# Optimization experiments

Measured on AMD Instinct MI355X. Metric: run time of the kernel, lower is better.

## Reference

```python
import jax, jax.numpy as jnp
import numpy as np

B, S, D, E, H = 8, 1024, 1024, 8, 4096  # batch, seq, n_embd, num_experts, 4*n_embd


def setup_inputs() -> dict:
    key = jax.random.key(0)
    ks = jax.random.split(key, 8)
    sc = 0.02
    return {
        "x": jax.random.normal(ks[0], (B, S, D), jnp.float32),
        "noise": jax.random.normal(ks[1], (B, S, E), jnp.float32),
        "Wg": jax.random.normal(ks[2], (D, E), jnp.float32) * sc,
        "bg": jnp.zeros((E,), jnp.float32),
        "Wn": jax.random.normal(ks[3], (D, E), jnp.float32) * sc,
        "bn": jnp.zeros((E,), jnp.float32),
        "W1": jax.random.normal(ks[4], (E, D, H), jnp.float32) * sc,
        "b1": jnp.zeros((E, H), jnp.float32),
        "W2": jax.random.normal(ks[5], (E, H, D), jnp.float32) * sc,
        "b2": jnp.zeros((E, D), jnp.float32),
        "top_k": 2,
    }


def reference(x, noise, Wg, bg, Wn, bn, W1, b1, W2, b2, top_k):
    # --- NoisyTopkRouter ---
    logits = jnp.einsum("bsd,de->bse", x, Wg) + bg
    noise_logits = jnp.einsum("bsd,de->bse", x, Wn) + bn
    noisy = logits + noise * jax.nn.softplus(noise_logits)  # [B,S,E]
    _, idx = jax.lax.top_k(noisy, top_k)  # [B,S,K]
    in_topk = jax.nn.one_hot(idx, noisy.shape[-1], dtype=noisy.dtype).sum(-2) > 0
    sparse_logits = jnp.where(in_topk, noisy, -jnp.inf)
    gating = jax.nn.softmax(sparse_logits, axis=-1)  # zero outside top-k

    # --- dispatch/combine: gating is exactly zero for non-selected experts,
    # so per-expert masked gather + weighted scatter-add == gated dense sum ---
    g_e = jnp.moveaxis(gating, -1, 0)  # [E,B,S]

    def body(acc, params):
        W1e, b1e, W2e, b2e, ge = params
        h = jax.nn.relu(jnp.einsum("bsd,dh->bsh", x, W1e) + b1e)  # [B,S,H]
        y = (jnp.einsum("bsh,hd->bsd", h, W2e) + b2e) * ge[..., None]
        return acc + y, y

    final_output, expert_outputs = jax.lax.scan(
        body, jnp.zeros_like(x), (W1, b1, W2, b2, g_e)
    )
    # expert_outputs: [E,B,S,D], matching the per-expert weighted outputs list
    return final_output, expert_outputs, gating
```

## Files before the change

kernel.cpp:

```cpp
#include <hip/hip_runtime.h>
#include <hip/hip_bf16.h>
#include <stdint.h>

#define TKN   8192
#define DD    1024
#define EE    8
#define HH    4096
#define TOPK  2
#define NASG  (TKN * TOPK)

typedef unsigned short u16;
typedef __bf16 bf16x8 __attribute__((ext_vector_type(8)));
typedef float  f32x4  __attribute__((ext_vector_type(4)));

__device__ __forceinline__ u16 f2bf(float f) {
  __hip_bfloat16 h = __float2bfloat16(f);
  return __builtin_bit_cast(u16, h);
}

__device__ __forceinline__ void glds16(const void* g, void* l) {
  __builtin_amdgcn_global_load_lds(
      (__attribute__((address_space(1))) void*)g,
      (__attribute__((address_space(3))) void*)l, 16, 0, 0);
}

#define FENCE() asm volatile("" ::: "memory")
#define BAR()   do { FENCE(); __builtin_amdgcn_s_barrier(); FENCE(); } while (0)
#define VMCNT4() asm volatile("s_waitcnt vmcnt(4)" ::: "memory")
#define VMCNT0() asm volatile("s_waitcnt vmcnt(0)" ::: "memory")

__global__ __launch_bounds__(256) void transpose_cvt_kernel(
    const float* __restrict__ src, u16* __restrict__ dst, int R, int C) {
  __shared__ float tile[32][33];
  int e = blockIdx.z;
  int c0 = blockIdx.x * 32, r0 = blockIdx.y * 32;
  int tx = threadIdx.x, ty = threadIdx.y;
  const float* s = src + (size_t)e * R * C;
  u16* d = dst + (size_t)e * R * C;
#pragma unroll
  for (int j = 0; j < 4; j++)
    tile[ty * 4 + j][tx] = s[(size_t)(r0 + ty * 4 + j) * C + c0 + tx];
  __syncthreads();
#pragma unroll
  for (int j = 0; j < 4; j++)
    d[(size_t)(c0 + ty * 4 + j) * R + r0 + tx] = f2bf(tile[tx][ty * 4 + j]);
}

__global__ __launch_bounds__(256) void router_kernel(
    const float* __restrict__ x, const float* __restrict__ noise,
    const float* __restrict__ Wg, const float* __restrict__ bg,
    const float* __restrict__ Wn, const float* __restrict__ bn,
    float* __restrict__ gating, u16* __restrict__ xb,
    int* __restrict__ sel_e, float* __restrict__ sel_g) {
  int t = blockIdx.x;
  int tid = threadIdx.x;
  float acc[16];
#pragma unroll
  for (int j = 0; j < 16; j++) acc[j] = 0.f;
  for (int i = tid; i < DD; i += 256) {
    float xv = x[(size_t)t * DD + i];
    xb[(size_t)t * DD + i] = f2bf(xv);
    const float4* g4 = (const float4*)(Wg + (size_t)i * EE);
    const float4* n4 = (const float4*)(Wn + (size_t)i * EE);
    float4 ga = g4[0], gb = g4[1];
    float4 na = n4[0], nb = n4[1];
    acc[0] += xv * ga.x;  acc[1] += xv * ga.y;  acc[2] += xv * ga.z;  acc[3] += xv * ga.w;
    acc[4] += xv * gb.x;  acc[5] += xv * gb.y;  acc[6] += xv * gb.z;  acc[7] += xv * gb.w;
    acc[8] += xv * na.x;  acc[9] += xv * na.y;  acc[10] += xv * na.z; acc[11] += xv * na.w;
    acc[12] += xv * nb.x; acc[13] += xv * nb.y; acc[14] += xv * nb.z; acc[15] += xv * nb.w;
  }
  __shared__ float red[4][16];
  int lane = tid & 63, wv = tid >> 6;
#pragma unroll
  for (int j = 0; j < 16; j++) {
    float v = acc[j];
    for (int o = 32; o > 0; o >>= 1) v += __shfl_down(v, o);
    acc[j] = v;
  }
  if (lane == 0) {
#pragma unroll
    for (int j = 0; j < 16; j++) red[wv][j] = acc[j];
  }
  __syncthreads();
  if (tid == 0) {
    float nz[EE];
#pragma unroll
    for (int e = 0; e < EE; e++) {
      float dg = red[0][e] + red[1][e] + red[2][e] + red[3][e] + bg[e];
      float dn = red[0][8 + e] + red[1][8 + e] + red[2][8 + e] + red[3][8 + e] + bn[e];
      float sp = fmaxf(dn, 0.f) + log1pf(expf(-fabsf(dn)));
      nz[e] = dg + noise[(size_t)t * EE + e] * sp;
    }
    int m1 = 0;
    for (int e = 1; e < EE; e++) if (nz[e] > nz[m1]) m1 = e;
    int m2 = (m1 == 0) ? 1 : 0;
    for (int e = 0; e < EE; e++) if (e != m1 && nz[e] > nz[m2]) m2 = e;
    float eb = expf(nz[m2] - nz[m1]);
    float den = 1.f + eb;
    float g1 = 1.f / den, g2 = eb / den;
    gating[(size_t)t * EE + m1] = g1;
    gating[(size_t)t * EE + m2] = g2;
    sel_e[t * 2] = m1; sel_e[t * 2 + 1] = m2;
    sel_g[t * 2] = g1; sel_g[t * 2 + 1] = g2;
  }
}

__global__ __launch_bounds__(256) void hist_scan_kernel(
    const int* __restrict__ sel_e, int* __restrict__ counts,
    int* __restrict__ offsets, int* __restrict__ cursors) {
  __shared__ int hist[EE];
  int tid = threadIdx.x;
  if (tid < EE) hist[tid] = 0;
  __syncthreads();
  for (int i = tid; i < NASG; i += 256) atomicAdd(&hist[sel_e[i]], 1);
  __syncthreads();
  if (tid == 0) {
    int off = 0;
    for (int e = 0; e < EE; e++) {
      counts[e] = hist[e]; offsets[e] = off; cursors[e] = off; off += hist[e];
    }
  }
}

__global__ __launch_bounds__(256) void build_lists_kernel(
    const int* __restrict__ sel_e, const float* __restrict__ sel_g,
    int* __restrict__ cursors, int* __restrict__ tok_list,
    float* __restrict__ gate_list) {
  int t = blockIdx.x * 256 + threadIdx.x;
  int lane = threadIdx.x & 63;
#pragma unroll
  for (int k = 0; k < TOPK; k++) {
    int e = sel_e[t * 2 + k];
    float g = sel_g[t * 2 + k];
    for (int ee = 0; ee < EE; ee++) {
      unsigned long long m = __ballot(e == ee);
      if (m) {
        int leader = __ffsll(m) - 1;
        int base = 0;
        if (lane == leader) base = atomicAdd(&cursors[ee], __popcll(m));
        base = __shfl(base, leader);
        if (e == ee) {
          int slot = base + __popcll(m & ((1ull << lane) - 1ull));
          tok_list[slot] = t;
          gate_list[slot] = g;
        }
      }
    }
  }
}

template<int KLEN, bool GATHER, bool EPI2>
__global__ __launch_bounds__(512, 2) void gemm8_kernel(
    const u16* __restrict__ A, const u16* __restrict__ Bm,
    const float* __restrict__ bias, const int* __restrict__ tok_list,
    const float* __restrict__ gate_list, const int* __restrict__ counts,
    const int* __restrict__ offsets, int Ncols,
    u16* __restrict__ OutBf, float* __restrict__ final_out,
    float* __restrict__ expert_out) {
  constexpr int NT = KLEN / 64;
  static_assert(KLEN % 64 == 0, "");
  int e = blockIdx.z;
  int cnt = counts[e];
  int rt = blockIdx.y;
  if (rt * 256 >= cnt) return;
  int off = offsets[e];
  int col0 = blockIdx.x * 256;

  __shared__ __attribute__((aligned(16))) char ldsc[131072];

  int tid = threadIdx.x;
  int w = tid >> 6, l = tid & 63;
  int wm = w >> 2, wn = w & 3;
  int fr = l & 15, hi = l >> 4;
  int kk16 = hi << 4;
  int xr = (fr & 7) << 4;

  int rl0 = w * 8 + (l >> 3);
  int slotE = ((l & 7) ^ ((l >> 3) & 7)) << 3;
  const u16* aptr[4];
  const u16* bptr[4];
#pragma unroll
  for (int i = 0; i < 4; i++) {
    int r = rt * 256 + rl0 + i * 64;
    if (GATHER) {
      int idx = min(off + r, NASG - 1);
      aptr[i] = A + (size_t)tok_list[idx] * KLEN + slotE;
    } else {
      aptr[i] = A + (size_t)(off + r) * KLEN + slotE;
    }
    bptr[i] = Bm + ((size_t)e * Ncols + col0 + rl0 + i * 64) * KLEN + slotE;
  }
  char* ldsA = ldsc;
  char* ldsB = ldsc + 65536;

  auto issueA = [&](int t, int h) {
    char* d = ldsA + (t & 1) * 32768 + h * 16384 + w * 1024;
    glds16(aptr[h * 2 + 0] + t * 64, d);
    glds16(aptr[h * 2 + 1] + t * 64, d + 8192);
  };
  auto issueB = [&](int t, int h) {
    char* d = ldsB + (t & 1) * 32768 + h * 16384 + w * 1024;
    glds16(bptr[h * 2 + 0] + t * 64, d);
    glds16(bptr[h * 2 + 1] + t * 64, d + 8192);
  };

  f32x4 acc[8][4];
#pragma unroll
  for (int m = 0; m < 8; m++)
#pragma unroll
    for (int n = 0; n < 4; n++) acc[m][n] = (f32x4){0.f, 0.f, 0.f, 0.f};
  bf16x8 aF[4][2], bF0[2][2], bF1[2][2];

  issueB(0, 0); issueB(0, 1); issueA(0, 0); issueA(0, 1);
  if (NT > 1) { issueB(1, 0); issueB(1, 1); }
  VMCNT4();
  BAR();

  for (int t = 0; t < NT; t++) {
    int abase = (t & 1) * 32768;
    int bbase = 65536 + (t & 1) * 32768;
#pragma unroll
    for (int mm = 0; mm < 4; mm++)
#pragma unroll
      for (int ks = 0; ks < 2; ks++)
        aF[mm][ks] = *(const bf16x8*)(ldsc + abase + (wm * 128 + mm * 16 + fr) * 128 +
                                      ((ks * 64 + kk16) ^ xr));
#pragma unroll
    for (int nn = 0; nn < 2; nn++)
#pragma unroll
      for (int ks = 0; ks < 2; ks++)
        bF0[nn][ks] = *(const bf16x8*)(ldsc + bbase + (wn * 64 + nn * 16 + fr) * 128 +
                                       ((ks * 64 + kk16) ^ xr));
    if (t + 1 < NT) issueA(t + 1, 0);
    BAR();
    __builtin_amdgcn_s_setprio(1);
#pragma unroll
    for (int mm = 0; mm < 4; mm++)
#pragma unroll
      for (int nn = 0; nn < 2; nn++)
#pragma unroll
        for (int ks = 0; ks < 2; ks++)
          acc[mm][nn] = __builtin_amdgcn_mfma_f32_16x16x32_bf16(aF[mm][ks], bF0[nn][ks], acc[mm][nn], 0, 0, 0);
    __builtin_amdgcn_s_setprio(0);
    BAR();
#pragma unroll
    for (int nn = 0; nn < 2; nn++)
#pragma unroll
      for (int ks = 0; ks < 2; ks++)
        bF1[nn][ks] = *(const bf16x8*)(ldsc + bbase + (wn * 64 + 32 + nn * 16 + fr) * 128 +
                                       ((ks * 64 + kk16) ^ xr));
    if (t + 1 < NT) issueA(t + 1, 1);
    BAR();
    __builtin_amdgcn_s_setprio(1);
#pragma unroll
    for (int mm = 0; mm < 4; mm++)
#pragma unroll
      for (int nn = 0; nn < 2; nn++)
#pragma unroll
        for (int ks = 0; ks < 2; ks++)
          acc[mm][2 + nn] = __builtin_amdgcn_mfma_f32_16x16x32_bf16(aF[mm][ks], bF1[nn][ks], acc[mm][2 + nn], 0, 0, 0);
    __builtin_amdgcn_s_setprio(0);
    BAR();
#pragma unroll
    for (int mm = 0; mm < 4; mm++)
#pragma unroll
      for (int ks = 0; ks < 2; ks++)
        aF[mm][ks] = *(const bf16x8*)(ldsc + abase + (wm * 128 + 64 + mm * 16 + fr) * 128 +
                                      ((ks * 64 + kk16) ^ xr));
    if (t + 2 < NT) issueB(t + 2, 0);
    BAR();
    __builtin_amdgcn_s_setprio(1);
#pragma unroll
    for (int mm = 0; mm < 4; mm++)
#pragma unroll
      for (int nn = 0; nn < 2; nn++)
#pragma unroll
        for (int ks = 0; ks < 2; ks++)
          acc[4 + mm][nn] = __builtin_amdgcn_mfma_f32_16x16x32_bf16(aF[mm][ks], bF0[nn][ks], acc[4 + mm][nn], 0, 0, 0);
    __builtin_amdgcn_s_setprio(0);
    BAR();
    if (t + 2 < NT) {
      issueB(t + 2, 1);
      VMCNT4();
    } else {
      VMCNT0();
    }
    BAR();
    __builtin_amdgcn_s_setprio(1);
#pragma unroll
    for (int mm = 0; mm < 4; mm++)
#pragma unroll
      for (int nn = 0; nn < 2; nn++)
#pragma unroll
        for (int ks = 0; ks < 2; ks++)
          acc[4 + mm][2 + nn] = __builtin_amdgcn_mfma_f32_16x16x32_bf16(aF[mm][ks], bF1[nn][ks], acc[4 + mm][2 + nn], 0, 0, 0);
    __builtin_amdgcn_s_setprio(0);
    BAR();
  }

  float biasN[4];
  int cN[4];
#pragma unroll
  for (int n = 0; n < 4; n++) {
    cN[n] = col0 + wn * 64 + (n >> 1) * 32 + (n & 1) * 16 + fr;
    biasN[n] = bias[e * Ncols + cN[n]];
  }
  if constexpr (!EPI2) {
#pragma unroll
    for (int m = 0; m < 8; m++) {
      int rb = rt * 256 + wm * 128 + (m >> 2) * 64 + (m & 3) * 16 + hi * 4;
#pragma unroll
      for (int j = 0; j < 4; j++) {
        int r = rb + j;
        if (r < cnt) {
#pragma unroll
          for (int n = 0; n < 4; n++) {
            float v = acc[m][n][j] + biasN[n];
            OutBf[(size_t)(off + r) * Ncols + cN[n]] = f2bf(fmaxf(v, 0.f));
          }
        }
      }
    }
  } else {
#pragma unroll
    for (int m = 0; m < 8; m++) {
      int rb = rt * 256 + wm * 128 + (m >> 2) * 64 + (m & 3) * 16 + hi * 4;
#pragma unroll
      for (int j = 0; j < 4; j++) {
        int r = rb + j;
        if (r < cnt) {
          int idx = off + r;
          int tok = tok_list[idx];
          float g = gate_list[idx];
          size_t erow = ((size_t)e * TKN + tok) * DD;
          size_t frow = (size_t)tok * DD;
#pragma unroll
          for (int n = 0; n < 4; n++) {
            float val = (acc[m][n][j] + biasN[n]) * g;
            expert_out[erow + cN[n]] = val;
            atomicAdd(&final_out[frow + cN[n]], val);
          }
        }
      }
    }
  }
}

extern "C" void kernel_launch(void* const* d_in, const int* in_sizes, int n_in,
                              void* d_out, int out_size, void* d_ws, size_t ws_size,
                              hipStream_t stream) {
  const float* x     = (const float*)d_in[0];
  const float* noise = (const float*)d_in[1];
  const float* Wg    = (const float*)d_in[2];
  const float* bg    = (const float*)d_in[3];
  const float* Wn    = (const float*)d_in[4];
  const float* bn    = (const float*)d_in[5];
  const float* W1    = (const float*)d_in[6];
  const float* b1    = (const float*)d_in[7];
  const float* W2    = (const float*)d_in[8];
  const float* b2    = (const float*)d_in[9];

  float* final_out  = (float*)d_out;
  float* expert_out = final_out + (size_t)TKN * DD;
  float* gating     = expert_out + (size_t)EE * TKN * DD;

  char* ws = (char*)d_ws;
  size_t o = 0;
  auto alloc = [&](size_t bytes) {
    char* p = ws + o;
    o += bytes;
    o = (o + 255) & ~(size_t)255;
    return p;
  };
  u16*   xb        = (u16*)alloc((size_t)TKN * DD * 2);
  u16*   w1t       = (u16*)alloc((size_t)EE * HH * DD * 2);
  u16*   w2t       = (u16*)alloc((size_t)EE * DD * HH * 2);
  u16*   hbuf      = (u16*)alloc(((size_t)NASG + 256) * HH * 2);
  int*   tok_list  = (int*)alloc((size_t)NASG * 4);
  float* gate_list = (float*)alloc((size_t)NASG * 4);
  int*   sel_e     = (int*)alloc((size_t)NASG * 4);
  float* sel_g     = (float*)alloc((size_t)NASG * 4);
  int*   counts    = (int*)alloc(256);
  int*   offsets   = (int*)alloc(256);
  int*   cursors   = (int*)alloc(256);

  hipMemsetAsync(d_out, 0, (size_t)out_size * sizeof(float), stream);

  transpose_cvt_kernel<<<dim3(HH / 32, DD / 32, EE), dim3(32, 8), 0, stream>>>(W1, w1t, DD, HH);
  transpose_cvt_kernel<<<dim3(DD / 32, HH / 32, EE), dim3(32, 8), 0, stream>>>(W2, w2t, HH, DD);

  router_kernel<<<TKN, 256, 0, stream>>>(x, noise, Wg, bg, Wn, bn, gating, xb, sel_e, sel_g);
  hist_scan_kernel<<<1, 256, 0, stream>>>(sel_e, counts, offsets, cursors);
  build_lists_kernel<<<TKN / 256, 256, 0, stream>>>(sel_e, sel_g, cursors, tok_list, gate_list);

  gemm8_kernel<DD, true, false><<<dim3(HH / 256, 64, EE), 512, 0, stream>>>(
      xb, w1t, b1, tok_list, nullptr, counts, offsets, HH, hbuf, nullptr, nullptr);
  gemm8_kernel<HH, false, true><<<dim3(DD / 256, 64, EE), 512, 0, stream>>>(
      hbuf, w2t, b2, tok_list, gate_list, counts, offsets, DD, nullptr, final_out, expert_out);
}
```

Measured before the change: 654.6 us.

## Compact grouped GEMM grid with slot table, drop atomics, deepen prefetch

The router and list building now run first and emit a compact list of (expert, row-tile) slots, so the GEMM grids launch only live tiles, in an XCD-interleaved order, instead of a sparse 3D grid full of early-exit blocks. The atomicAdd into final_out is removed. A combine kernel now sums each token's two expert rows, and a zerofill kernel writes zeros only to unselected expert rows rather than memsetting the whole output. The A-tile prefetch moves two stages ahead alongside B, waiting on vmcnt(8), which gives more latency hiding at the cost of extra outstanding loads. NSLOT=72 assumes at most 72 live tiles; that holds under balanced routing but could overflow if routing is heavily skewed.

```diff
diff --git a/kernel.cpp b/kernel.cpp
--- a/kernel.cpp
+++ b/kernel.cpp
@@ -8,6 +8,7 @@
 #define HH    4096
 #define TOPK  2
 #define NASG  (TKN * TOPK)
+#define NSLOT 72
 
 typedef unsigned short u16;
 typedef __bf16 bf16x8 __attribute__((ext_vector_type(8)));
@@ -26,7 +27,7 @@
 
 #define FENCE() asm volatile("" ::: "memory")
 #define BAR()   do { FENCE(); __builtin_amdgcn_s_barrier(); FENCE(); } while (0)
-#define VMCNT4() asm volatile("s_waitcnt vmcnt(4)" ::: "memory")
+#define VMCNT8() asm volatile("s_waitcnt vmcnt(8)" ::: "memory")
 #define VMCNT0() asm volatile("s_waitcnt vmcnt(0)" ::: "memory")
 
 __global__ __launch_bounds__(256) void transpose_cvt_kernel(
@@ -107,7 +108,8 @@
 
 __global__ __launch_bounds__(256) void hist_scan_kernel(
     const int* __restrict__ sel_e, int* __restrict__ counts,
-    int* __restrict__ offsets, int* __restrict__ cursors) {
+    int* __restrict__ offsets, int* __restrict__ cursors,
+    int* __restrict__ slots) {
   __shared__ int hist[EE];
   int tid = threadIdx.x;
   if (tid < EE) hist[tid] = 0;
@@ -115,10 +117,14 @@
   for (int i = tid; i < NASG; i += 256) atomicAdd(&hist[sel_e[i]], 1);
   __syncthreads();
   if (tid == 0) {
-    int off = 0;
+    int off = 0, ns = 0;
     for (int e = 0; e < EE; e++) {
-      counts[e] = hist[e]; offsets[e] = off; cursors[e] = off; off += hist[e];
-    }
+      int c = hist[e];
+      counts[e] = c; offsets[e] = off; cursors[e] = off; off += c;
+      int nrt = (c + 255) >> 8;
+      for (int rt = 0; rt < nrt; rt++) slots[ns++] = (e << 16) | rt;
+    }
+    for (; ns < NSLOT; ns++) slots[ns] = -1;
   }
 }
 
@@ -149,22 +155,47 @@
   }
 }
 
-template<int KLEN, bool GATHER, bool EPI2>
+__global__ __launch_bounds__(256) void zerofill_kernel(
+    const float* __restrict__ gating, float* __restrict__ expert_out) {
+  int id = blockIdx.x;
+  int e = id >> 13, t = id & (TKN - 1);
+  if (gating[(size_t)t * EE + e] != 0.f) return;
+  float4* p = (float4*)(expert_out + ((size_t)e * TKN + t) * DD);
+  p[threadIdx.x] = (float4){0.f, 0.f, 0.f, 0.f};
+}
+
+__global__ __launch_bounds__(256) void combine_kernel(
+    const float* __restrict__ expert_out, const int* __restrict__ sel_e,
+    float* __restrict__ final_out) {
+  int t = blockIdx.x;
+  int e1 = sel_e[2 * t], e2 = sel_e[2 * t + 1];
+  const float4* r1 = (const float4*)(expert_out + ((size_t)e1 * TKN + t) * DD);
+  const float4* r2 = (const float4*)(expert_out + ((size_t)e2 * TKN + t) * DD);
+  float4* o = (float4*)(final_out + (size_t)t * DD);
+  int i = threadIdx.x;
+  float4 a = r1[i], b = r2[i];
+  o[i] = (float4){a.x + b.x, a.y + b.y, a.z + b.z, a.w + b.w};
+}
+
+template<int KLEN, bool GATHER, bool EPI2, int LOGC>
 __global__ __launch_bounds__(512, 2) void gemm8_kernel(
     const u16* __restrict__ A, const u16* __restrict__ Bm,
     const float* __restrict__ bias, const int* __restrict__ tok_list,
     const float* __restrict__ gate_list, const int* __restrict__ counts,
-    const int* __restrict__ offsets, int Ncols,
-    u16* __restrict__ OutBf, float* __restrict__ final_out,
-    float* __restrict__ expert_out) {
+    const int* __restrict__ offsets, const int* __restrict__ slots,
+    int Ncols, u16* __restrict__ OutBf, float* __restrict__ expert_out) {
   constexpr int NT = KLEN / 64;
-  static_assert(KLEN % 64 == 0, "");
-  int e = blockIdx.z;
+  int gid = blockIdx.x;
+  int q = gid >> 3;
+  int slot = (gid & 7) * 9 + (q >> LOGC);
+  int ct = q & ((1 << LOGC) - 1);
+  int packed = slots[slot];
+  if (packed < 0) return;
+  int e = packed >> 16;
+  int rt = packed & 0xffff;
   int cnt = counts[e];
-  int rt = blockIdx.y;
-  if (rt * 256 >= cnt) return;
   int off = offsets[e];
-  int col0 = blockIdx.x * 256;
+  int col0 = ct * 256;
 
   __shared__ __attribute__((aligned(16))) char ldsc[131072];
 
@@ -212,8 +243,8 @@
   bf16x8 aF[4][2], bF0[2][2], bF1[2][2];
 
   issueB(0, 0); issueB(0, 1); issueA(0, 0); issueA(0, 1);
-  if (NT > 1) { issueB(1, 0); issueB(1, 1); }
-  VMCNT4();
+  issueB(1, 0); issueB(1, 1); issueA(1, 0); issueA(1, 1);
+  VMCNT8();
   BAR();
 
   for (int t = 0; t < NT; t++) {
@@ -231,7 +262,6 @@
       for (int ks = 0; ks < 2; ks++)
         bF0[nn][ks] = *(const bf16x8*)(ldsc + bbase + (wn * 64 + nn * 16 + fr) * 128 +
                                        ((ks * 64 + kk16) ^ xr));
-    if (t + 1 < NT) issueA(t + 1, 0);
     BAR();
     __builtin_amdgcn_s_setprio(1);
 #pragma unroll
@@ -249,7 +279,6 @@
       for (int ks = 0; ks < 2; ks++)
         bF1[nn][ks] = *(const bf16x8*)(ldsc + bbase + (wn * 64 + 32 + nn * 16 + fr) * 128 +
                                        ((ks * 64 + kk16) ^ xr));
-    if (t + 1 < NT) issueA(t + 1, 1);
     BAR();
     __builtin_amdgcn_s_setprio(1);
 #pragma unroll
@@ -267,7 +296,7 @@
       for (int ks = 0; ks < 2; ks++)
         aF[mm][ks] = *(const bf16x8*)(ldsc + abase + (wm * 128 + 64 + mm * 16 + fr) * 128 +
                                       ((ks * 64 + kk16) ^ xr));
-    if (t + 2 < NT) issueB(t + 2, 0);
+    if (t + 2 < NT) { issueB(t + 2, 0); issueB(t + 2, 1); }
     BAR();
     __builtin_amdgcn_s_setprio(1);
 #pragma unroll
@@ -280,8 +309,8 @@
     __builtin_amdgcn_s_setprio(0);
     BAR();
     if (t + 2 < NT) {
-      issueB(t + 2, 1);
-      VMCNT4();
+      issueA(t + 2, 0); issueA(t + 2, 1);
+      VMCNT8();
     } else {
       VMCNT0();
     }
@@ -333,13 +362,9 @@
           int tok = tok_list[idx];
           float g = gate_list[idx];
           size_t erow = ((size_t)e * TKN + tok) * DD;
-          size_t frow = (size_t)tok * DD;
-#pragma unroll
-          for (int n = 0; n < 4; n++) {
-            float val = (acc[m][n][j] + biasN[n]) * g;
-            expert_out[erow + cN[n]] = val;
-            atomicAdd(&final_out[frow + cN[n]], val);
-          }
+#pragma unroll
+          for (int n = 0; n < 4; n++)
+            expert_out[erow + cN[n]] = (acc[m][n][j] + biasN[n]) * g;
         }
       }
     }
@@ -383,18 +408,22 @@
   int*   counts    = (int*)alloc(256);
   int*   offsets   = (int*)alloc(256);
   int*   cursors   = (int*)alloc(256);
-
-  hipMemsetAsync(d_out, 0, (size_t)out_size * sizeof(float), stream);
+  int*   slots     = (int*)alloc(NSLOT * 4);
+
+  hipMemsetAsync(gating, 0, (size_t)TKN * EE * sizeof(float), stream);
+
+  router_kernel<<<TKN, 256, 0, stream>>>(x, noise, Wg, bg, Wn, bn, gating, xb, sel_e, sel_g);
+  hist_scan_kernel<<<1, 256, 0, stream>>>(sel_e, counts, offsets, cursors, slots);
+  build_lists_kernel<<<TKN / 256, 256, 0, stream>>>(sel_e, sel_g, cursors, tok_list, gate_list);
+  zerofill_kernel<<<EE * TKN, 256, 0, stream>>>(gating, expert_out);
 
   transpose_cvt_kernel<<<dim3(HH / 32, DD / 32, EE), dim3(32, 8), 0, stream>>>(W1, w1t, DD, HH);
   transpose_cvt_kernel<<<dim3(DD / 32, HH / 32, EE), dim3(32, 8), 0, stream>>>(W2, w2t, HH, DD);
 
-  router_kernel<<<TKN, 256, 0, stream>>>(x, noise, Wg, bg, Wn, bn, gating, xb, sel_e, sel_g);
-  hist_scan_kernel<<<1, 256, 0, stream>>>(sel_e, counts, offsets, cursors);
-  build_lists_kernel<<<TKN / 256, 256, 0, stream>>>(sel_e, sel_g, cursors, tok_list, gate_list);
-
-  gemm8_kernel<DD, true, false><<<dim3(HH / 256, 64, EE), 512, 0, stream>>>(
-      xb, w1t, b1, tok_list, nullptr, counts, offsets, HH, hbuf, nullptr, nullptr);
-  gemm8_kernel<HH, false, true><<<dim3(DD / 256, 64, EE), 512, 0, stream>>>(
-      hbuf, w2t, b2, tok_list, gate_list, counts, offsets, DD, nullptr, final_out, expert_out);
-}
+  gemm8_kernel<DD, true, false, 4><<<8 * 9 * 16, 512, 0, stream>>>(
+      xb, w1t, b1, tok_list, nullptr, counts, offsets, slots, HH, hbuf, nullptr);
+  gemm8_kernel<HH, false, true, 2><<<8 * 9 * 4, 512, 0, stream>>>(
+      hbuf, w2t, b2, tok_list, gate_list, counts, offsets, slots, DD, nullptr, expert_out);
+
+  combine_kernel<<<TKN, 256, 0, stream>>>(expert_out, sel_e, final_out);
+}
```

New measurement: 670.5 us. 1.02x slower.
